# Performance work log

Hardware: AMD Instinct MI355X
Metric: run time of the kernel (lower is better)

Reference implementation:

```python
import jax, jax.numpy as jnp
import numpy as np

C_IN = 256
K = 4
C_QK = C_IN // K  # 64


def setup_inputs() -> dict:
    key = jax.random.key(0)
    ks = jax.random.split(key, 9)
    B, C, H, W = 4, C_IN, 64, 64
    s = 0.02
    return {
        "x": jax.random.normal(ks[0], (B, C, H, W), dtype=jnp.float32),
        # 1x1 convs stored as dense [out, in] matrices (kernel_size=1)
        "wq": jax.random.normal(ks[1], (C_QK, C), dtype=jnp.float32) * s,
        "bq": jax.random.normal(ks[2], (C_QK,), dtype=jnp.float32) * s,
        "wk": jax.random.normal(ks[3], (C_QK, C), dtype=jnp.float32) * s,
        "bk": jax.random.normal(ks[4], (C_QK,), dtype=jnp.float32) * s,
        "wv": jax.random.normal(ks[5], (C, C), dtype=jnp.float32) * s,
        "bv": jax.random.normal(ks[6], (C,), dtype=jnp.float32) * s,
        "wg": jax.random.normal(ks[7], (C, C), dtype=jnp.float32) * s,
        "bg": jax.random.normal(ks[8], (C,), dtype=jnp.float32) * s,
    }


def reference(x, wq, bq, wk, bk, wv, bv, wg, bg):
    B, C, H, W = x.shape
    N = H * W
    xf = x.reshape(B, C, N)  # [B, C, N]
    # 1x1 conv == per-pixel linear over channels
    q = jnp.einsum("oc,bcn->bon", wq, xf) + bq[None, :, None]  # [B, Cqk, N]
    k = jnp.einsum("oc,bcn->bon", wk, xf) + bk[None, :, None]  # [B, Cqk, N]
    v = jnp.einsum("oc,bcn->bon", wv, xf) + bv[None, :, None]  # [B, C, N]
    # energy[b, n, m] = <q[:, n], k[:, m]>  (n = query pos, m = key pos)
    energy = jnp.einsum("bon,bom->bnm", q, k)  # [B, N, N]
    energy = jax.nn.elu(energy) / N
    # out[b, c, m] = sum_n v[b, c, n] * energy[b, n, m]
    out = jnp.einsum("bcn,bnm->bcm", v, energy).reshape(B, C, H, W)
    out = jnp.einsum("oc,bchw->bohw", wg, out) + bg[None, :, None, None]
    return out
```

## Files before the change

### kernel.cpp

```cpp
#include <hip/hip_runtime.h>

#define B_ 4
#define C_ 256
#define CQK 64
#define N_ 4096
#define SEG 2
#define SEGN (N_ / SEG)
#define NB 128
#define ITERS (SEGN / NB)
#define TS 512

typedef _Float16 f16;
typedef __attribute__((ext_vector_type(8))) _Float16 f16x8;
typedef __attribute__((ext_vector_type(4))) _Float16 f16x4;
typedef __attribute__((ext_vector_type(4))) float f32x4;

#define TILE_OFF(l15, quad) ((l15) * 32 + (quad) * 8)

__global__ __launch_bounds__(256) void prep(
    const float* __restrict__ x, const float* __restrict__ wq,
    const float* __restrict__ wk, const float* __restrict__ wv,
    const float* __restrict__ wg, f16* __restrict__ xtt, f16* __restrict__ WQt,
    f16* __restrict__ WKt, f16* __restrict__ WVt, f16* __restrict__ WGt) {
  __shared__ float tile[64][65];
  if (blockIdx.x < 64) {
    int n0 = blockIdx.x * 64, c0 = blockIdx.y * 64, b = blockIdx.z;
    const float* xb = x + (size_t)b * C_ * N_;
    int lane = threadIdx.x & 63;
    int grp = threadIdx.x >> 6;
#pragma unroll
    for (int i = 0; i < 16; i++) {
      int c = grp * 16 + i;
      tile[lane][c] = xb[(size_t)(c0 + c) * N_ + n0 + lane];
    }
    __syncthreads();
    f16* xtb = xtt + (size_t)b * N_ * C_;
    int ti = threadIdx.x >> 6;
    int l15 = threadIdx.x & 15;
    int qq = (threadIdx.x >> 4) & 3;
    int nl = ti * 16 + l15;
    size_t tb = ((size_t)((n0 >> 4) + ti) * 8 + (c0 >> 5) + (qq >> 1)) * TS;
    f16* dst = xtb + tb + l15 * 32 + (qq & 1) * 16;
    f16x8 v0, v1;
#pragma unroll
    for (int j = 0; j < 8; j++) v0[j] = (f16)tile[nl][qq * 16 + j];
#pragma unroll
    for (int j = 0; j < 8; j++) v1[j] = (f16)tile[nl][qq * 16 + 8 + j];
    *(f16x8*)dst = v0;
    *(f16x8*)(dst + 8) = v1;
  } else {
    int wid = (((blockIdx.x - 64) * 16) + blockIdx.z * 4 + blockIdx.y) * 256 +
              threadIdx.x;
    for (int chunk = wid; chunk < 20480; chunk += 16384) {
      const float* src;
      f16* dst;
      int lo;
      if (chunk < 2048) { src = wq; dst = WQt; lo = chunk * 8; }
      else if (chunk < 4096) { src = wk; dst = WKt; lo = (chunk - 2048) * 8; }
      else if (chunk < 12288) { src = wv; dst = WVt; lo = (chunk - 4096) * 8; }
      else { src = wg; dst = WGt; lo = (chunk - 12288) * 8; }
      int o = lo >> 8, k = lo & 255;
      f16x8 v;
#pragma unroll
      for (int j = 0; j < 8; j++) v[j] = (f16)src[lo + j];
      *(f16x8*)(dst + ((size_t)(o >> 4) * 8 + (k >> 5)) * TS + (o & 15) * 32 +
                (k & 31)) = v;
    }
  }
}

__global__ __launch_bounds__(256) void proj_all(
    const f16* __restrict__ WQt, const f16* __restrict__ WKt,
    const f16* __restrict__ WVt, const float* __restrict__ bq,
    const float* __restrict__ bk, const float* __restrict__ bv,
    const f16* __restrict__ xtt, f16* __restrict__ QTt, f16* __restrict__ KTt,
    f16* __restrict__ Vt) {
  int n0 = blockIdx.x * 64;
  int y = blockIdx.y;
  int b = blockIdx.z;
  int tid = threadIdx.x, lane = tid & 63, w = tid >> 6;
  int l15 = lane & 15, quad = lane >> 4;
  const f16* xtb = xtt + (size_t)b * N_ * C_;
  if (y < 2) {
    const f16* Wt = y ? WKt : WQt;
    const float* bias = y ? bk : bq;
    f16* outT = y ? KTt : QTt;
    f32x4 acc[4];
#pragma unroll
    for (int nt = 0; nt < 4; nt++) acc[nt] = (f32x4){0.f, 0.f, 0.f, 0.f};
#pragma unroll
    for (int kt = 0; kt < 8; kt++) {
      f16x8 a = *(const f16x8*)(Wt + ((size_t)w * 8 + kt) * TS + TILE_OFF(l15, quad));
#pragma unroll
      for (int nt = 0; nt < 4; nt++) {
        f16x8 bf = *(const f16x8*)(xtb + ((size_t)((n0 >> 4) + nt) * 8 + kt) * TS +
                                   TILE_OFF(l15, quad));
        acc[nt] = __builtin_amdgcn_mfma_f32_16x16x32_f16(a, bf, acc[nt], 0, 0, 0);
      }
    }
    f16* ob = outT + (size_t)b * N_ * CQK;
    int o_lo = 16 * (w & 1) + 4 * quad;
    int okt = w >> 1;
#pragma unroll
    for (int nt = 0; nt < 4; nt++) {
      f16x4 vals;
#pragma unroll
      for (int r = 0; r < 4; r++)
        vals[r] = (f16)(acc[nt][r] + bias[16 * w + 4 * quad + r]);
      *(f16x4*)(ob + ((size_t)((n0 >> 4) + nt) * 2 + okt) * TS + l15 * 32 + o_lo) =
          vals;
    }
  } else {
    int o0 = (y - 2) * 64;
    f32x4 acc[4];
#pragma unroll
    for (int ot = 0; ot < 4; ot++) acc[ot] = (f32x4){0.f, 0.f, 0.f, 0.f};
#pragma unroll
    for (int kt = 0; kt < 8; kt++) {
      f16x8 a = *(const f16x8*)(xtb + ((size_t)((n0 >> 4) + w) * 8 + kt) * TS +
                                TILE_OFF(l15, quad));
#pragma unroll
      for (int ot = 0; ot < 4; ot++) {
        f16x8 bb = *(const f16x8*)(WVt + ((size_t)((o0 >> 4) + ot) * 8 + kt) * TS +
                                   TILE_OFF(l15, quad));
        acc[ot] = __builtin_amdgcn_mfma_f32_16x16x32_f16(a, bb, acc[ot], 0, 0, 0);
      }
    }
    f16* vbout = Vt + (size_t)b * C_ * N_;
    int n_lo = 16 * (w & 1) + 4 * quad;
    int ntile = (n0 >> 5) + (w >> 1);
#pragma unroll
    for (int ot = 0; ot < 4; ot++) {
      float bvv = bv[o0 + 16 * ot + l15];
      f16x4 vals;
#pragma unroll
      for (int r = 0; r < 4; r++) vals[r] = (f16)(acc[ot][r] + bvv);
      *(f16x4*)(vbout + ((size_t)((o0 >> 4) + ot) * 128 + ntile) * TS + l15 * 32 +
                n_lo) = vals;
    }
  }
}

__global__ __launch_bounds__(256, 2) void attn(const f16* __restrict__ qt,
                                               const f16* __restrict__ kt,
                                               const f16* __restrict__ v,
                                               f16* __restrict__ oT) {
  __shared__ __align__(16) f16 sPt[2][64][128];
  int m0 = blockIdx.x * 64;
  int seg = blockIdx.y;
  int b = blockIdx.z;
  int tid = threadIdx.x, lane = tid & 63, w = tid >> 6;
  int l15 = lane & 15, quad = lane >> 4;
  const f16* qtb = qt + (size_t)b * N_ * CQK;
  const f16* ktb = kt + (size_t)b * N_ * CQK;
  const f16* vb = v + (size_t)b * C_ * N_;

  f32x4 oacc[4][4];
#pragma unroll
  for (int ct = 0; ct < 4; ct++)
#pragma unroll
    for (int mt = 0; mt < 4; mt++) oacc[ct][mt] = (f32x4){0.f, 0.f, 0.f, 0.f};

  f16x8 kf[4][2];
#pragma unroll
  for (int mt = 0; mt < 4; mt++)
#pragma unroll
    for (int ks = 0; ks < 2; ks++)
      kf[mt][ks] = *(const f16x8*)(ktb + ((size_t)((m0 >> 4) + mt) * 2 + ks) * TS +
                                   TILE_OFF(l15, quad));

  f16x8 qf[2][2];
  {
    int nq = seg * SEGN;
#pragma unroll
    for (int nt = 0; nt < 2; nt++)
#pragma unroll
      for (int ks = 0; ks < 2; ks++)
        qf[nt][ks] = *(const f16x8*)(qtb +
                                     ((size_t)((nq >> 4) + 2 * w + nt) * 2 + ks) * TS +
                                     TILE_OFF(l15, quad));
  }

  for (int it = 0; it < ITERS; it++) {
    int n0 = seg * SEGN + it * NB;
    f16x8 vfA[2][4];
#pragma unroll
    for (int ks = 0; ks < 2; ks++)
#pragma unroll
      for (int ct = 0; ct < 4; ct++)
        vfA[ks][ct] = *(const f16x8*)(vb +
                                      ((size_t)(4 * w + ct) * 128 + (n0 >> 5) + ks) * TS +
                                      TILE_OFF(l15, quad));

    char* buf = (char*)sPt[it & 1];
#pragma unroll
    for (int nt = 0; nt < 2; nt++) {
      f32x4 sacc[4];
#pragma unroll
      for (int mt = 0; mt < 4; mt++) sacc[mt] = (f32x4){0.f, 0.f, 0.f, 0.f};
#pragma unroll
      for (int ks = 0; ks < 2; ks++)
#pragma unroll
        for (int mt = 0; mt < 4; mt++)
          sacc[mt] = __builtin_amdgcn_mfma_f32_16x16x32_f16(qf[nt][ks], kf[mt][ks],
                                                            sacc[mt], 0, 0, 0);
#pragma unroll
      for (int mt = 0; mt < 4; mt++) {
        f16x4 p;
#pragma unroll
        for (int r = 0; r < 4; r++) {
          float s = sacc[mt][r];
          p[r] = (f16)(s > 0.0f ? s : (__expf(s) - 1.0f));
        }
        int row = 16 * mt + l15;
        int colb = (64 * w + 32 * nt + 8 * quad) ^ ((row & 7) << 4);
        *(f16x4*)(buf + row * 256 + colb) = p;
      }
    }
    __syncthreads();

    f16x8 vfB[2][4];
    f16x8 pa[4];
#pragma unroll
    for (int mt = 0; mt < 4; mt++) {
      int row = 16 * mt + l15;
      int colb = (quad * 16) ^ ((row & 7) << 4);
      pa[mt] = *(const f16x8*)(buf + row * 256 + colb);
    }
#pragma unroll
    for (int ks = 0; ks < 2; ks++)
#pragma unroll
      for (int ct = 0; ct < 4; ct++)
        vfB[ks][ct] = *(const f16x8*)(vb + ((size_t)(4 * w + ct) * 128 + (n0 >> 5) +
                                            2 + ks) * TS +
                                      TILE_OFF(l15, quad));
#pragma unroll
    for (int ct = 0; ct < 4; ct++)
#pragma unroll
      for (int mt = 0; mt < 4; mt++)
        oacc[ct][mt] = __builtin_amdgcn_mfma_f32_16x16x32_f16(vfA[0][ct], pa[mt],
                                                              oacc[ct][mt], 0, 0, 0);
    if (it + 1 < ITERS) {
      int nq = n0 + NB;
#pragma unroll
      for (int nt = 0; nt < 2; nt++)
#pragma unroll
        for (int ks = 0; ks < 2; ks++)
          qf[nt][ks] = *(const f16x8*)(qtb +
                                       ((size_t)((nq >> 4) + 2 * w + nt) * 2 + ks) * TS +
                                       TILE_OFF(l15, quad));
    }
#pragma unroll
    for (int mt = 0; mt < 4; mt++) {
      int row = 16 * mt + l15;
      pa[mt] = *(const f16x8*)(buf + row * 256 + ((64 + quad * 16) ^ ((row & 7) << 4)));
    }
#pragma unroll
    for (int ct = 0; ct < 4; ct++)
#pragma unroll
      for (int mt = 0; mt < 4; mt++)
        oacc[ct][mt] = __builtin_amdgcn_mfma_f32_16x16x32_f16(vfA[1][ct], pa[mt],
                                                              oacc[ct][mt], 0, 0, 0);
#pragma unroll
    for (int mt = 0; mt < 4; mt++) {
      int row = 16 * mt + l15;
      pa[mt] = *(const f16x8*)(buf + row * 256 + ((128 + quad * 16) ^ ((row & 7) << 4)));
    }
#pragma unroll
    for (int ct = 0; ct < 4; ct++)
#pragma unroll
      for (int mt = 0; mt < 4; mt++)
        oacc[ct][mt] = __builtin_amdgcn_mfma_f32_16x16x32_f16(vfB[0][ct], pa[mt],
                                                              oacc[ct][mt], 0, 0, 0);
#pragma unroll
    for (int mt = 0; mt < 4; mt++) {
      int row = 16 * mt + l15;
      pa[mt] = *(const f16x8*)(buf + row * 256 + ((192 + quad * 16) ^ ((row & 7) << 4)));
    }
#pragma unroll
    for (int ct = 0; ct < 4; ct++)
#pragma unroll
      for (int mt = 0; mt < 4; mt++)
        oacc[ct][mt] = __builtin_amdgcn_mfma_f32_16x16x32_f16(vfB[1][ct], pa[mt],
                                                              oacc[ct][mt], 0, 0, 0);
  }

  f16* ob = oT + ((size_t)seg * B_ + b) * N_ * C_;
#pragma unroll
  for (int ct = 0; ct < 4; ct++) {
#pragma unroll
    for (int mt = 0; mt < 4; mt++) {
      f16x4 vals;
#pragma unroll
      for (int r = 0; r < 4; r++)
        vals[r] = (f16)(oacc[ct][mt][r] * (1.0f / (float)N_));
      size_t tb = ((size_t)((m0 >> 4) + mt) * 8 + 2 * w + (ct >> 1)) * TS;
      *(f16x4*)(ob + tb + l15 * 32 + 16 * (ct & 1) + 4 * quad) = vals;
    }
  }
}

__global__ __launch_bounds__(256) void final_proj(const f16* __restrict__ WGt,
                                                  const float* __restrict__ bias,
                                                  const f16* __restrict__ ot,
                                                  float* __restrict__ out) {
  int m0 = blockIdx.x * 64, o0 = blockIdx.y * 64, b = blockIdx.z;
  int tid = threadIdx.x, lane = tid & 63, w = tid >> 6;
  int l15 = lane & 15, quad = lane >> 4;
  const f16* otb0 = ot + (size_t)b * N_ * C_;
  const f16* otb1 = ot + ((size_t)B_ + b) * N_ * C_;
  f32x4 acc[4];
#pragma unroll
  for (int mt = 0; mt < 4; mt++) acc[mt] = (f32x4){0.f, 0.f, 0.f, 0.f};
#pragma unroll
  for (int kt = 0; kt < 8; kt++) {
    f16x8 a = *(const f16x8*)(WGt + ((size_t)((o0 >> 4) + w) * 8 + kt) * TS +
                              TILE_OFF(l15, quad));
#pragma unroll
    for (int mt = 0; mt < 4; mt++) {
      size_t off = ((size_t)((m0 >> 4) + mt) * 8 + kt) * TS + TILE_OFF(l15, quad);
      f16x8 b0 = *(const f16x8*)(otb0 + off);
      f16x8 b1 = *(const f16x8*)(otb1 + off);
      f16x8 bb = b0 + b1;
      acc[mt] = __builtin_amdgcn_mfma_f32_16x16x32_f16(a, bb, acc[mt], 0, 0, 0);
    }
  }
  float* outb = out + (size_t)b * C_ * N_;
  int ol = o0 + 16 * w + quad * 4;
#pragma unroll
  for (int mt = 0; mt < 4; mt++) {
    int m = m0 + 16 * mt + l15;
#pragma unroll
    for (int r = 0; r < 4; r++)
      outb[(size_t)(ol + r) * N_ + m] = acc[mt][r] + bias[ol + r];
  }
}

extern "C" void kernel_launch(void* const* d_in, const int* in_sizes, int n_in,
                              void* d_out, int out_size, void* d_ws, size_t ws_size,
                              hipStream_t stream) {
  const float* x = (const float*)d_in[0];
  const float* wq = (const float*)d_in[1];
  const float* bq = (const float*)d_in[2];
  const float* wk = (const float*)d_in[3];
  const float* bk = (const float*)d_in[4];
  const float* wv = (const float*)d_in[5];
  const float* bv = (const float*)d_in[6];
  const float* wg = (const float*)d_in[7];
  const float* bg = (const float*)d_in[8];
  float* out = (float*)d_out;

  char* ws = (char*)d_ws;
  f16* OTt = (f16*)ws;
  f16* XTt = (f16*)ws;
  ws += (size_t)SEG * B_ * N_ * C_ * sizeof(f16);
  f16* QTt = (f16*)ws; ws += (size_t)B_ * N_ * CQK * sizeof(f16);
  f16* KTt = (f16*)ws; ws += (size_t)B_ * N_ * CQK * sizeof(f16);
  f16* Vt  = (f16*)ws; ws += (size_t)B_ * C_ * N_ * sizeof(f16);
  f16* WQt = (f16*)ws; ws += (size_t)CQK * C_ * sizeof(f16);
  f16* WKt = (f16*)ws; ws += (size_t)CQK * C_ * sizeof(f16);
  f16* WVt = (f16*)ws; ws += (size_t)C_ * C_ * sizeof(f16);
  f16* WGt = (f16*)ws; ws += (size_t)C_ * C_ * sizeof(f16);

  prep<<<dim3(68, 4, 4), 256, 0, stream>>>(x, wq, wk, wv, wg, XTt, WQt, WKt, WVt, WGt);
  proj_all<<<dim3(N_ / 64, 6, B_), 256, 0, stream>>>(WQt, WKt, WVt, bq, bk, bv,
                                                     XTt, QTt, KTt, Vt);
  attn<<<dim3(N_ / 64, SEG, B_), 256, 0, stream>>>(QTt, KTt, Vt, OTt);
  final_proj<<<dim3(N_ / 64, C_ / 64, B_), 256, 0, stream>>>(WGt, bg, OTt, out);
}
```

Measured before the change: 172.8 us.

## Fuse transpose into projection and output projection into attention kernel

Replaces four launches with two. The fp32 transpose/cast of x moves into the projection kernel through shared memory, and one block now computes Q, K and V for its pixel tile. The attention kernel drops the split-N segmentation, halves its key-tile width to 32 so the grid stays large, and applies the wg output projection in-kernel from LDS. This removes the intermediate workspace round-trips and the segment-sum pass. In exchange, weights are converted from fp32 per block instead of once, and each attention block carries the full N loop with smaller MFMA tiles.

```diff
diff --git a/kernel.cpp b/kernel.cpp
--- a/kernel.cpp
+++ b/kernel.cpp
@@ -4,10 +4,8 @@
 #define C_ 256
 #define CQK 64
 #define N_ 4096
-#define SEG 2
-#define SEGN (N_ / SEG)
 #define NB 128
-#define ITERS (SEGN / NB)
+#define ITERS (N_ / NB)
 #define TS 512
 
 typedef _Float16 f16;
@@ -17,126 +15,105 @@
 
 #define TILE_OFF(l15, quad) ((l15) * 32 + (quad) * 8)
 
-__global__ __launch_bounds__(256) void prep(
+__global__ __launch_bounds__(256) void proj(
     const float* __restrict__ x, const float* __restrict__ wq,
-    const float* __restrict__ wk, const float* __restrict__ wv,
-    const float* __restrict__ wg, f16* __restrict__ xtt, f16* __restrict__ WQt,
-    f16* __restrict__ WKt, f16* __restrict__ WVt, f16* __restrict__ WGt) {
-  __shared__ float tile[64][65];
-  if (blockIdx.x < 64) {
-    int n0 = blockIdx.x * 64, c0 = blockIdx.y * 64, b = blockIdx.z;
-    const float* xb = x + (size_t)b * C_ * N_;
-    int lane = threadIdx.x & 63;
-    int grp = threadIdx.x >> 6;
-#pragma unroll
-    for (int i = 0; i < 16; i++) {
-      int c = grp * 16 + i;
-      tile[lane][c] = xb[(size_t)(c0 + c) * N_ + n0 + lane];
-    }
-    __syncthreads();
-    f16* xtb = xtt + (size_t)b * N_ * C_;
-    int ti = threadIdx.x >> 6;
-    int l15 = threadIdx.x & 15;
-    int qq = (threadIdx.x >> 4) & 3;
-    int nl = ti * 16 + l15;
-    size_t tb = ((size_t)((n0 >> 4) + ti) * 8 + (c0 >> 5) + (qq >> 1)) * TS;
-    f16* dst = xtb + tb + l15 * 32 + (qq & 1) * 16;
-    f16x8 v0, v1;
-#pragma unroll
-    for (int j = 0; j < 8; j++) v0[j] = (f16)tile[nl][qq * 16 + j];
-#pragma unroll
-    for (int j = 0; j < 8; j++) v1[j] = (f16)tile[nl][qq * 16 + 8 + j];
-    *(f16x8*)dst = v0;
-    *(f16x8*)(dst + 8) = v1;
-  } else {
-    int wid = (((blockIdx.x - 64) * 16) + blockIdx.z * 4 + blockIdx.y) * 256 +
-              threadIdx.x;
-    for (int chunk = wid; chunk < 20480; chunk += 16384) {
-      const float* src;
-      f16* dst;
-      int lo;
-      if (chunk < 2048) { src = wq; dst = WQt; lo = chunk * 8; }
-      else if (chunk < 4096) { src = wk; dst = WKt; lo = (chunk - 2048) * 8; }
-      else if (chunk < 12288) { src = wv; dst = WVt; lo = (chunk - 4096) * 8; }
-      else { src = wg; dst = WGt; lo = (chunk - 12288) * 8; }
-      int o = lo >> 8, k = lo & 255;
-      f16x8 v;
-#pragma unroll
-      for (int j = 0; j < 8; j++) v[j] = (f16)src[lo + j];
-      *(f16x8*)(dst + ((size_t)(o >> 4) * 8 + (k >> 5)) * TS + (o & 15) * 32 +
-                (k & 31)) = v;
-    }
-  }
-}
-
-__global__ __launch_bounds__(256) void proj_all(
-    const f16* __restrict__ WQt, const f16* __restrict__ WKt,
-    const f16* __restrict__ WVt, const float* __restrict__ bq,
-    const float* __restrict__ bk, const float* __restrict__ bv,
-    const f16* __restrict__ xtt, f16* __restrict__ QTt, f16* __restrict__ KTt,
+    const float* __restrict__ bq, const float* __restrict__ wk,
+    const float* __restrict__ bk, const float* __restrict__ wv,
+    const float* __restrict__ bv, f16* __restrict__ QTt, f16* __restrict__ KTt,
     f16* __restrict__ Vt) {
+  __shared__ float xs[64][65];
+  __shared__ f16 xt[4 * 8 * TS];
   int n0 = blockIdx.x * 64;
-  int y = blockIdx.y;
-  int b = blockIdx.z;
+  int b = blockIdx.y;
   int tid = threadIdx.x, lane = tid & 63, w = tid >> 6;
   int l15 = lane & 15, quad = lane >> 4;
-  const f16* xtb = xtt + (size_t)b * N_ * C_;
-  if (y < 2) {
-    const f16* Wt = y ? WKt : WQt;
-    const float* bias = y ? bk : bq;
-    f16* outT = y ? KTt : QTt;
-    f32x4 acc[4];
-#pragma unroll
-    for (int nt = 0; nt < 4; nt++) acc[nt] = (f32x4){0.f, 0.f, 0.f, 0.f};
-#pragma unroll
-    for (int kt = 0; kt < 8; kt++) {
-      f16x8 a = *(const f16x8*)(Wt + ((size_t)w * 8 + kt) * TS + TILE_OFF(l15, quad));
-#pragma unroll
-      for (int nt = 0; nt < 4; nt++) {
-        f16x8 bf = *(const f16x8*)(xtb + ((size_t)((n0 >> 4) + nt) * 8 + kt) * TS +
-                                   TILE_OFF(l15, quad));
-        acc[nt] = __builtin_amdgcn_mfma_f32_16x16x32_f16(a, bf, acc[nt], 0, 0, 0);
-      }
-    }
-    f16* ob = outT + (size_t)b * N_ * CQK;
-    int o_lo = 16 * (w & 1) + 4 * quad;
-    int okt = w >> 1;
+  const float* xb = x + (size_t)b * C_ * N_;
+
+  for (int cc = 0; cc < 4; cc++) {
+#pragma unroll
+    for (int i = 0; i < 16; i++)
+      xs[lane][w * 16 + i] = xb[(size_t)(cc * 64 + w * 16 + i) * N_ + n0 + lane];
+    __syncthreads();
+    {
+      int nt = w;
+      f16x8 v0, v1;
+#pragma unroll
+      for (int j = 0; j < 8; j++) v0[j] = (f16)xs[nt * 16 + l15][quad * 16 + j];
+#pragma unroll
+      for (int j = 0; j < 8; j++) v1[j] = (f16)xs[nt * 16 + l15][quad * 16 + 8 + j];
+      f16* dst = xt + (nt * 8 + cc * 2 + (quad >> 1)) * TS + l15 * 32 + (quad & 1) * 16;
+      *(f16x8*)dst = v0;
+      *(f16x8*)(dst + 8) = v1;
+    }
+    __syncthreads();
+  }
+
+  const float* wqk = (w < 2) ? wq : wk;
+  const float* bqk = (w < 2) ? bq : bk;
+  f32x4 accV[4][4];
+  f32x4 accQ[2][4];
+#pragma unroll
+  for (int ot = 0; ot < 4; ot++)
+#pragma unroll
+    for (int nt = 0; nt < 4; nt++) accV[ot][nt] = (f32x4){0.f, 0.f, 0.f, 0.f};
+#pragma unroll
+  for (int ot = 0; ot < 2; ot++)
+#pragma unroll
+    for (int nt = 0; nt < 4; nt++) accQ[ot][nt] = (f32x4){0.f, 0.f, 0.f, 0.f};
+
+#pragma unroll
+  for (int kt = 0; kt < 8; kt++) {
+    f16x8 xf[4];
+#pragma unroll
+    for (int nt = 0; nt < 4; nt++)
+      xf[nt] = *(const f16x8*)(xt + (nt * 8 + kt) * TS + TILE_OFF(l15, quad));
+#pragma unroll
+    for (int ot = 0; ot < 4; ot++) {
+      const float* p = wv + (size_t)(64 * w + 16 * ot + l15) * C_ + kt * 32 + quad * 8;
+      f16x8 bf;
+#pragma unroll
+      for (int j = 0; j < 8; j++) bf[j] = (f16)p[j];
+#pragma unroll
+      for (int nt = 0; nt < 4; nt++)
+        accV[ot][nt] = __builtin_amdgcn_mfma_f32_16x16x32_f16(xf[nt], bf, accV[ot][nt], 0, 0, 0);
+    }
+#pragma unroll
+    for (int ot = 0; ot < 2; ot++) {
+      const float* p = wqk + (size_t)(32 * (w & 1) + 16 * ot + l15) * C_ + kt * 32 + quad * 8;
+      f16x8 af;
+#pragma unroll
+      for (int j = 0; j < 8; j++) af[j] = (f16)p[j];
+#pragma unroll
+      for (int nt = 0; nt < 4; nt++)
+        accQ[ot][nt] = __builtin_amdgcn_mfma_f32_16x16x32_f16(af, xf[nt], accQ[ot][nt], 0, 0, 0);
+    }
+  }
+
+  f16* vbout = Vt + (size_t)b * C_ * N_;
+#pragma unroll
+  for (int ot = 0; ot < 4; ot++) {
+    int o = 64 * w + 16 * ot + l15;
+    float bvv = bv[o];
 #pragma unroll
     for (int nt = 0; nt < 4; nt++) {
       f16x4 vals;
 #pragma unroll
+      for (int r = 0; r < 4; r++) vals[r] = (f16)(accV[ot][nt][r] + bvv);
+      *(f16x4*)(vbout + ((size_t)(4 * w + ot) * 128 + (n0 >> 5) + (nt >> 1)) * TS +
+                l15 * 32 + 16 * (nt & 1) + 4 * quad) = vals;
+    }
+  }
+  f16* ob = ((w < 2) ? QTt : KTt) + (size_t)b * N_ * CQK;
+#pragma unroll
+  for (int ot = 0; ot < 2; ot++) {
+#pragma unroll
+    for (int nt = 0; nt < 4; nt++) {
+      f16x4 vals;
+#pragma unroll
       for (int r = 0; r < 4; r++)
-        vals[r] = (f16)(acc[nt][r] + bias[16 * w + 4 * quad + r]);
-      *(f16x4*)(ob + ((size_t)((n0 >> 4) + nt) * 2 + okt) * TS + l15 * 32 + o_lo) =
-          vals;
-    }
-  } else {
-    int o0 = (y - 2) * 64;
-    f32x4 acc[4];
-#pragma unroll
-    for (int ot = 0; ot < 4; ot++) acc[ot] = (f32x4){0.f, 0.f, 0.f, 0.f};
-#pragma unroll
-    for (int kt = 0; kt < 8; kt++) {
-      f16x8 a = *(const f16x8*)(xtb + ((size_t)((n0 >> 4) + w) * 8 + kt) * TS +
-                                TILE_OFF(l15, quad));
-#pragma unroll
-      for (int ot = 0; ot < 4; ot++) {
-        f16x8 bb = *(const f16x8*)(WVt + ((size_t)((o0 >> 4) + ot) * 8 + kt) * TS +
-                                   TILE_OFF(l15, quad));
-        acc[ot] = __builtin_amdgcn_mfma_f32_16x16x32_f16(a, bb, acc[ot], 0, 0, 0);
-      }
-    }
-    f16* vbout = Vt + (size_t)b * C_ * N_;
-    int n_lo = 16 * (w & 1) + 4 * quad;
-    int ntile = (n0 >> 5) + (w >> 1);
-#pragma unroll
-    for (int ot = 0; ot < 4; ot++) {
-      float bvv = bv[o0 + 16 * ot + l15];
-      f16x4 vals;
-#pragma unroll
-      for (int r = 0; r < 4; r++) vals[r] = (f16)(acc[ot][r] + bvv);
-      *(f16x4*)(vbout + ((size_t)((o0 >> 4) + ot) * 128 + ntile) * TS + l15 * 32 +
-                n_lo) = vals;
+        vals[r] = (f16)(accQ[ot][nt][r] + bqk[32 * (w & 1) + 16 * ot + 4 * quad + r]);
+      *(f16x4*)(ob + (((size_t)(n0 >> 4) + nt) * 2 + (w & 1)) * TS + l15 * 32 +
+                16 * ot + 4 * quad) = vals;
     }
   }
 }
@@ -144,45 +121,42 @@
 __global__ __launch_bounds__(256, 2) void attn(const f16* __restrict__ qt,
                                                const f16* __restrict__ kt,
                                                const f16* __restrict__ v,
-                                               f16* __restrict__ oT) {
-  __shared__ __align__(16) f16 sPt[2][64][128];
-  int m0 = blockIdx.x * 64;
-  int seg = blockIdx.y;
-  int b = blockIdx.z;
+                                               const float* __restrict__ wg,
+                                               const float* __restrict__ bg,
+                                               float* __restrict__ out) {
+  __shared__ __align__(16) f16 sPt[2][32][128];
+  int m0 = blockIdx.x * 32;
+  int b = blockIdx.y;
   int tid = threadIdx.x, lane = tid & 63, w = tid >> 6;
   int l15 = lane & 15, quad = lane >> 4;
   const f16* qtb = qt + (size_t)b * N_ * CQK;
   const f16* ktb = kt + (size_t)b * N_ * CQK;
   const f16* vb = v + (size_t)b * C_ * N_;
 
-  f32x4 oacc[4][4];
+  f32x4 oacc[4][2];
 #pragma unroll
   for (int ct = 0; ct < 4; ct++)
 #pragma unroll
-    for (int mt = 0; mt < 4; mt++) oacc[ct][mt] = (f32x4){0.f, 0.f, 0.f, 0.f};
-
-  f16x8 kf[4][2];
-#pragma unroll
-  for (int mt = 0; mt < 4; mt++)
+    for (int mt = 0; mt < 2; mt++) oacc[ct][mt] = (f32x4){0.f, 0.f, 0.f, 0.f};
+
+  f16x8 kf[2][2];
+#pragma unroll
+  for (int mt = 0; mt < 2; mt++)
 #pragma unroll
     for (int ks = 0; ks < 2; ks++)
       kf[mt][ks] = *(const f16x8*)(ktb + ((size_t)((m0 >> 4) + mt) * 2 + ks) * TS +
                                    TILE_OFF(l15, quad));
 
   f16x8 qf[2][2];
-  {
-    int nq = seg * SEGN;
-#pragma unroll
-    for (int nt = 0; nt < 2; nt++)
-#pragma unroll
-      for (int ks = 0; ks < 2; ks++)
-        qf[nt][ks] = *(const f16x8*)(qtb +
-                                     ((size_t)((nq >> 4) + 2 * w + nt) * 2 + ks) * TS +
-                                     TILE_OFF(l15, quad));
-  }
+#pragma unroll
+  for (int nt = 0; nt < 2; nt++)
+#pragma unroll
+    for (int ks = 0; ks < 2; ks++)
+      qf[nt][ks] = *(const f16x8*)(qtb + ((size_t)(2 * w + nt) * 2 + ks) * TS +
+                                   TILE_OFF(l15, quad));
 
   for (int it = 0; it < ITERS; it++) {
-    int n0 = seg * SEGN + it * NB;
+    int n0 = it * NB;
     f16x8 vfA[2][4];
 #pragma unroll
     for (int ks = 0; ks < 2; ks++)
@@ -195,17 +169,17 @@
     char* buf = (char*)sPt[it & 1];
 #pragma unroll
     for (int nt = 0; nt < 2; nt++) {
-      f32x4 sacc[4];
-#pragma unroll
-      for (int mt = 0; mt < 4; mt++) sacc[mt] = (f32x4){0.f, 0.f, 0.f, 0.f};
+      f32x4 sacc[2];
+#pragma unroll
+      for (int mt = 0; mt < 2; mt++) sacc[mt] = (f32x4){0.f, 0.f, 0.f, 0.f};
 #pragma unroll
       for (int ks = 0; ks < 2; ks++)
 #pragma unroll
-        for (int mt = 0; mt < 4; mt++)
+        for (int mt = 0; mt < 2; mt++)
           sacc[mt] = __builtin_amdgcn_mfma_f32_16x16x32_f16(qf[nt][ks], kf[mt][ks],
                                                             sacc[mt], 0, 0, 0);
 #pragma unroll
-      for (int mt = 0; mt < 4; mt++) {
+      for (int mt = 0; mt < 2; mt++) {
         f16x4 p;
 #pragma unroll
         for (int r = 0; r < 4; r++) {
@@ -220,12 +194,11 @@
     __syncthreads();
 
     f16x8 vfB[2][4];
-    f16x8 pa[4];
-#pragma unroll
-    for (int mt = 0; mt < 4; mt++) {
+    f16x8 pa[2];
+#pragma unroll
+    for (int mt = 0; mt < 2; mt++) {
       int row = 16 * mt + l15;
-      int colb = (quad * 16) ^ ((row & 7) << 4);
-      pa[mt] = *(const f16x8*)(buf + row * 256 + colb);
+      pa[mt] = *(const f16x8*)(buf + row * 256 + ((quad * 16) ^ ((row & 7) << 4)));
     }
 #pragma unroll
     for (int ks = 0; ks < 2; ks++)
@@ -237,7 +210,7 @@
 #pragma unroll
     for (int ct = 0; ct < 4; ct++)
 #pragma unroll
-      for (int mt = 0; mt < 4; mt++)
+      for (int mt = 0; mt < 2; mt++)
         oacc[ct][mt] = __builtin_amdgcn_mfma_f32_16x16x32_f16(vfA[0][ct], pa[mt],
                                                               oacc[ct][mt], 0, 0, 0);
     if (it + 1 < ITERS) {
@@ -251,88 +224,89 @@
                                        TILE_OFF(l15, quad));
     }
 #pragma unroll
-    for (int mt = 0; mt < 4; mt++) {
+    for (int mt = 0; mt < 2; mt++) {
       int row = 16 * mt + l15;
       pa[mt] = *(const f16x8*)(buf + row * 256 + ((64 + quad * 16) ^ ((row & 7) << 4)));
     }
 #pragma unroll
     for (int ct = 0; ct < 4; ct++)
 #pragma unroll
-      for (int mt = 0; mt < 4; mt++)
+      for (int mt = 0; mt < 2; mt++)
         oacc[ct][mt] = __builtin_amdgcn_mfma_f32_16x16x32_f16(vfA[1][ct], pa[mt],
                                                               oacc[ct][mt], 0, 0, 0);
 #pragma unroll
-    for (int mt = 0; mt < 4; mt++) {
+    for (int mt = 0; mt < 2; mt++) {
       int row = 16 * mt + l15;
       pa[mt] = *(const f16x8*)(buf + row * 256 + ((128 + quad * 16) ^ ((row & 7) << 4)));
     }
 #pragma unroll
     for (int ct = 0; ct < 4; ct++)
 #pragma unroll
-      for (int mt = 0; mt < 4; mt++)
+      for (int mt = 0; mt < 2; mt++)
         oacc[ct][mt] = __builtin_amdgcn_mfma_f32_16x16x32_f16(vfB[0][ct], pa[mt],
                                                               oacc[ct][mt], 0, 0, 0);
 #pragma unroll
-    for (int mt = 0; mt < 4; mt++) {
+    for (int mt = 0; mt < 2; mt++) {
       int row = 16 * mt + l15;
       pa[mt] = *(const f16x8*)(buf + row * 256 + ((192 + quad * 16) ^ ((row & 7) << 4)));
     }
 #pragma unroll
     for (int ct = 0; ct < 4; ct++)
 #pragma unroll
-      for (int mt = 0; mt < 4; mt++)
+      for (int mt = 0; mt < 2; mt++)
         oacc[ct][mt] = __builtin_amdgcn_mfma_f32_16x16x32_f16(vfB[1][ct], pa[mt],
                                                               oacc[ct][mt], 0, 0, 0);
   }
 
-  f16* ob = oT + ((size_t)seg * B_ + b) * N_ * C_;
+  __syncthreads();
+  f16* obuf = (f16*)sPt;
 #pragma unroll
   for (int ct = 0; ct < 4; ct++) {
 #pragma unroll
-    for (int mt = 0; mt < 4; mt++) {
+    for (int mt = 0; mt < 2; mt++) {
       f16x4 vals;
 #pragma unroll
       for (int r = 0; r < 4; r++)
         vals[r] = (f16)(oacc[ct][mt][r] * (1.0f / (float)N_));
-      size_t tb = ((size_t)((m0 >> 4) + mt) * 8 + 2 * w + (ct >> 1)) * TS;
-      *(f16x4*)(ob + tb + l15 * 32 + 16 * (ct & 1) + 4 * quad) = vals;
-    }
-  }
-}
-
-__global__ __launch_bounds__(256) void final_proj(const f16* __restrict__ WGt,
-                                                  const float* __restrict__ bias,
-                                                  const f16* __restrict__ ot,
-                                                  float* __restrict__ out) {
-  int m0 = blockIdx.x * 64, o0 = blockIdx.y * 64, b = blockIdx.z;
-  int tid = threadIdx.x, lane = tid & 63, w = tid >> 6;
-  int l15 = lane & 15, quad = lane >> 4;
-  const f16* otb0 = ot + (size_t)b * N_ * C_;
-  const f16* otb1 = ot + ((size_t)B_ + b) * N_ * C_;
-  f32x4 acc[4];
-#pragma unroll
-  for (int mt = 0; mt < 4; mt++) acc[mt] = (f32x4){0.f, 0.f, 0.f, 0.f};
+      *(f16x4*)(obuf + (mt * 8 + 2 * w + (ct >> 1)) * TS + l15 * 32 +
+                16 * (ct & 1) + 4 * quad) = vals;
+    }
+  }
+  __syncthreads();
+  f32x4 accO[4][2];
+#pragma unroll
+  for (int ot = 0; ot < 4; ot++)
+#pragma unroll
+    for (int mt = 0; mt < 2; mt++) accO[ot][mt] = (f32x4){0.f, 0.f, 0.f, 0.f};
 #pragma unroll
   for (int kt = 0; kt < 8; kt++) {
-    f16x8 a = *(const f16x8*)(WGt + ((size_t)((o0 >> 4) + w) * 8 + kt) * TS +
-                              TILE_OFF(l15, quad));
-#pragma unroll
-    for (int mt = 0; mt < 4; mt++) {
-      size_t off = ((size_t)((m0 >> 4) + mt) * 8 + kt) * TS + TILE_OFF(l15, quad);
-      f16x8 b0 = *(const f16x8*)(otb0 + off);
-      f16x8 b1 = *(const f16x8*)(otb1 + off);
-      f16x8 bb = b0 + b1;
-      acc[mt] = __builtin_amdgcn_mfma_f32_16x16x32_f16(a, bb, acc[mt], 0, 0, 0);
+    f16x8 bO[2];
+#pragma unroll
+    for (int mt = 0; mt < 2; mt++)
+      bO[mt] = *(const f16x8*)(obuf + (mt * 8 + kt) * TS + TILE_OFF(l15, quad));
+#pragma unroll
+    for (int ot = 0; ot < 4; ot++) {
+      const float* p = wg + (size_t)(64 * w + 16 * ot + l15) * C_ + kt * 32 + quad * 8;
+      f16x8 af;
+#pragma unroll
+      for (int j = 0; j < 8; j++) af[j] = (f16)p[j];
+#pragma unroll
+      for (int mt = 0; mt < 2; mt++)
+        accO[ot][mt] = __builtin_amdgcn_mfma_f32_16x16x32_f16(af, bO[mt], accO[ot][mt], 0, 0, 0);
     }
   }
   float* outb = out + (size_t)b * C_ * N_;
-  int ol = o0 + 16 * w + quad * 4;
-#pragma unroll
-  for (int mt = 0; mt < 4; mt++) {
-    int m = m0 + 16 * mt + l15;
-#pragma unroll
-    for (int r = 0; r < 4; r++)
-      outb[(size_t)(ol + r) * N_ + m] = acc[mt][r] + bias[ol + r];
+#pragma unroll
+  for (int ot = 0; ot < 4; ot++) {
+#pragma unroll
+    for (int mt = 0; mt < 2; mt++) {
+      int m = m0 + 16 * mt + l15;
+#pragma unroll
+      for (int r = 0; r < 4; r++) {
+        int o = 64 * w + 16 * ot + 4 * quad + r;
+        outb[(size_t)o * N_ + m] = accO[ot][mt][r] + bg[o];
+      }
+    }
   }
 }
 
@@ -351,20 +325,11 @@
   float* out = (float*)d_out;
 
   char* ws = (char*)d_ws;
-  f16* OTt = (f16*)ws;
-  f16* XTt = (f16*)ws;
-  ws += (size_t)SEG * B_ * N_ * C_ * sizeof(f16);
   f16* QTt = (f16*)ws; ws += (size_t)B_ * N_ * CQK * sizeof(f16);
   f16* KTt = (f16*)ws; ws += (size_t)B_ * N_ * CQK * sizeof(f16);
   f16* Vt  = (f16*)ws; ws += (size_t)B_ * C_ * N_ * sizeof(f16);
-  f16* WQt = (f16*)ws; ws += (size_t)CQK * C_ * sizeof(f16);
-  f16* WKt = (f16*)ws; ws += (size_t)CQK * C_ * sizeof(f16);
-  f16* WVt = (f16*)ws; ws += (size_t)C_ * C_ * sizeof(f16);
-  f16* WGt = (f16*)ws; ws += (size_t)C_ * C_ * sizeof(f16);
-
-  prep<<<dim3(68, 4, 4), 256, 0, stream>>>(x, wq, wk, wv, wg, XTt, WQt, WKt, WVt, WGt);
-  proj_all<<<dim3(N_ / 64, 6, B_), 256, 0, stream>>>(WQt, WKt, WVt, bq, bk, bv,
-                                                     XTt, QTt, KTt, Vt);
-  attn<<<dim3(N_ / 64, SEG, B_), 256, 0, stream>>>(QTt, KTt, Vt, OTt);
-  final_proj<<<dim3(N_ / 64, C_ / 64, B_), 256, 0, stream>>>(WGt, bg, OTt, out);
+
+  proj<<<dim3(N_ / 64, B_), 256, 0, stream>>>(x, wq, bq, wk, bk, wv, bv,
+                                              QTt, KTt, Vt);
+  attn<<<dim3(N_ / 32, B_), 256, 0, stream>>>(QTt, KTt, Vt, wg, bg, out);
 }
```

After: 202.1 us. +17.0%, slower.

## Fuse x transpose into projection and output projection into attention epilogue

Applied to the files above, without the earlier changes.

Splits weight conversion into its own small kernel, and moves the x transpose/f16 conversion into the projection kernel via shared memory. All Q, K and V tiles are now computed per 512-thread block, so the f16 transposed copy of x is no longer written to or read from global memory. The Wg projection is applied inside the attention epilogue on each segment's output, producing fp32 partials that a combine kernel sums and biases. This removes the intermediate f16 attention-output round trip and the separate final GEMM. In exchange it writes two full fp32 partial tensors and adds one more elementwise pass.

```diff
diff --git a/kernel.cpp b/kernel.cpp
--- a/kernel.cpp
+++ b/kernel.cpp
@@ -14,129 +14,118 @@
 typedef __attribute__((ext_vector_type(8))) _Float16 f16x8;
 typedef __attribute__((ext_vector_type(4))) _Float16 f16x4;
 typedef __attribute__((ext_vector_type(4))) float f32x4;
+typedef __attribute__((ext_vector_type(4))) float float4v;
 
 #define TILE_OFF(l15, quad) ((l15) * 32 + (quad) * 8)
 
-__global__ __launch_bounds__(256) void prep(
-    const float* __restrict__ x, const float* __restrict__ wq,
-    const float* __restrict__ wk, const float* __restrict__ wv,
-    const float* __restrict__ wg, f16* __restrict__ xtt, f16* __restrict__ WQt,
-    f16* __restrict__ WKt, f16* __restrict__ WVt, f16* __restrict__ WGt) {
-  __shared__ float tile[64][65];
-  if (blockIdx.x < 64) {
-    int n0 = blockIdx.x * 64, c0 = blockIdx.y * 64, b = blockIdx.z;
-    const float* xb = x + (size_t)b * C_ * N_;
-    int lane = threadIdx.x & 63;
-    int grp = threadIdx.x >> 6;
-#pragma unroll
-    for (int i = 0; i < 16; i++) {
-      int c = grp * 16 + i;
-      tile[lane][c] = xb[(size_t)(c0 + c) * N_ + n0 + lane];
-    }
-    __syncthreads();
-    f16* xtb = xtt + (size_t)b * N_ * C_;
-    int ti = threadIdx.x >> 6;
-    int l15 = threadIdx.x & 15;
-    int qq = (threadIdx.x >> 4) & 3;
-    int nl = ti * 16 + l15;
-    size_t tb = ((size_t)((n0 >> 4) + ti) * 8 + (c0 >> 5) + (qq >> 1)) * TS;
-    f16* dst = xtb + tb + l15 * 32 + (qq & 1) * 16;
-    f16x8 v0, v1;
-#pragma unroll
-    for (int j = 0; j < 8; j++) v0[j] = (f16)tile[nl][qq * 16 + j];
-#pragma unroll
-    for (int j = 0; j < 8; j++) v1[j] = (f16)tile[nl][qq * 16 + 8 + j];
-    *(f16x8*)dst = v0;
-    *(f16x8*)(dst + 8) = v1;
-  } else {
-    int wid = (((blockIdx.x - 64) * 16) + blockIdx.z * 4 + blockIdx.y) * 256 +
-              threadIdx.x;
-    for (int chunk = wid; chunk < 20480; chunk += 16384) {
-      const float* src;
-      f16* dst;
-      int lo;
-      if (chunk < 2048) { src = wq; dst = WQt; lo = chunk * 8; }
-      else if (chunk < 4096) { src = wk; dst = WKt; lo = (chunk - 2048) * 8; }
-      else if (chunk < 12288) { src = wv; dst = WVt; lo = (chunk - 4096) * 8; }
-      else { src = wg; dst = WGt; lo = (chunk - 12288) * 8; }
-      int o = lo >> 8, k = lo & 255;
-      f16x8 v;
-#pragma unroll
-      for (int j = 0; j < 8; j++) v[j] = (f16)src[lo + j];
-      *(f16x8*)(dst + ((size_t)(o >> 4) * 8 + (k >> 5)) * TS + (o & 15) * 32 +
-                (k & 31)) = v;
-    }
-  }
-}
-
-__global__ __launch_bounds__(256) void proj_all(
-    const f16* __restrict__ WQt, const f16* __restrict__ WKt,
-    const f16* __restrict__ WVt, const float* __restrict__ bq,
-    const float* __restrict__ bk, const float* __restrict__ bv,
-    const f16* __restrict__ xtt, f16* __restrict__ QTt, f16* __restrict__ KTt,
+__global__ __launch_bounds__(256) void prep_w(
+    const float* __restrict__ wq, const float* __restrict__ wk,
+    const float* __restrict__ wv, const float* __restrict__ wg,
+    f16* __restrict__ WQt, f16* __restrict__ WKt, f16* __restrict__ WVt,
+    f16* __restrict__ WGt) {
+  int chunk = blockIdx.x * 256 + threadIdx.x;
+  if (chunk >= 20480) return;
+  const float* src;
+  f16* dst;
+  int lo;
+  if (chunk < 2048) { src = wq; dst = WQt; lo = chunk * 8; }
+  else if (chunk < 4096) { src = wk; dst = WKt; lo = (chunk - 2048) * 8; }
+  else if (chunk < 12288) { src = wv; dst = WVt; lo = (chunk - 4096) * 8; }
+  else { src = wg; dst = WGt; lo = (chunk - 12288) * 8; }
+  int o = lo >> 8, k = lo & 255;
+  f16x8 v;
+#pragma unroll
+  for (int j = 0; j < 8; j++) v[j] = (f16)src[lo + j];
+  *(f16x8*)(dst + ((size_t)(o >> 4) * 8 + (k >> 5)) * TS + (o & 15) * 32 + (k & 31)) = v;
+}
+
+__global__ __launch_bounds__(512) void proj(
+    const float* __restrict__ x, const f16* __restrict__ WQt,
+    const f16* __restrict__ WKt, const f16* __restrict__ WVt,
+    const float* __restrict__ bq, const float* __restrict__ bk,
+    const float* __restrict__ bv, f16* __restrict__ QTt, f16* __restrict__ KTt,
     f16* __restrict__ Vt) {
+  __shared__ float xs[64][65];
+  __shared__ f16 xt[4 * 8 * TS];
   int n0 = blockIdx.x * 64;
-  int y = blockIdx.y;
-  int b = blockIdx.z;
+  int b = blockIdx.y;
   int tid = threadIdx.x, lane = tid & 63, w = tid >> 6;
   int l15 = lane & 15, quad = lane >> 4;
-  const f16* xtb = xtt + (size_t)b * N_ * C_;
-  if (y < 2) {
-    const f16* Wt = y ? WKt : WQt;
-    const float* bias = y ? bk : bq;
-    f16* outT = y ? KTt : QTt;
-    f32x4 acc[4];
-#pragma unroll
-    for (int nt = 0; nt < 4; nt++) acc[nt] = (f32x4){0.f, 0.f, 0.f, 0.f};
-#pragma unroll
-    for (int kt = 0; kt < 8; kt++) {
-      f16x8 a = *(const f16x8*)(Wt + ((size_t)w * 8 + kt) * TS + TILE_OFF(l15, quad));
+  const float* xb = x + (size_t)b * C_ * N_;
+
+  for (int cc = 0; cc < 4; cc++) {
+#pragma unroll
+    for (int i = 0; i < 8; i++)
+      xs[lane][w * 8 + i] = xb[(size_t)(cc * 64 + w * 8 + i) * N_ + n0 + lane];
+    __syncthreads();
+    {
+      int nt = w >> 1;
+      f16x8 v;
+#pragma unroll
+      for (int j = 0; j < 8; j++)
+        v[j] = (f16)xs[nt * 16 + l15][32 * (w & 1) + quad * 8 + j];
+      *(f16x8*)(xt + (nt * 8 + cc * 2 + (w & 1)) * TS + l15 * 32 + quad * 8) = v;
+    }
+    __syncthreads();
+  }
+
+  f32x4 acc[3][4];
+#pragma unroll
+  for (int j = 0; j < 3; j++)
+#pragma unroll
+    for (int nt = 0; nt < 4; nt++) acc[j][nt] = (f32x4){0.f, 0.f, 0.f, 0.f};
+
+#pragma unroll
+  for (int kt = 0; kt < 8; kt++) {
+    f16x8 xf[4];
+#pragma unroll
+    for (int nt = 0; nt < 4; nt++)
+      xf[nt] = *(const f16x8*)(xt + (nt * 8 + kt) * TS + TILE_OFF(l15, quad));
+#pragma unroll
+    for (int j = 0; j < 3; j++) {
+      int g = w * 3 + j;
+      const f16* Wt;
+      int ot;
+      bool isV = g < 16;
+      if (isV) { Wt = WVt; ot = g; }
+      else if (g < 20) { Wt = WQt; ot = g - 16; }
+      else { Wt = WKt; ot = g - 20; }
+      f16x8 wf = *(const f16x8*)(Wt + ((size_t)ot * 8 + kt) * TS + TILE_OFF(l15, quad));
+#pragma unroll
+      for (int nt = 0; nt < 4; nt++)
+        acc[j][nt] = isV
+            ? __builtin_amdgcn_mfma_f32_16x16x32_f16(xf[nt], wf, acc[j][nt], 0, 0, 0)
+            : __builtin_amdgcn_mfma_f32_16x16x32_f16(wf, xf[nt], acc[j][nt], 0, 0, 0);
+    }
+  }
+
+  f16* vbout = Vt + (size_t)b * C_ * N_;
+#pragma unroll
+  for (int j = 0; j < 3; j++) {
+    int g = w * 3 + j;
+    if (g < 16) {
+      float bvv = bv[16 * g + l15];
 #pragma unroll
       for (int nt = 0; nt < 4; nt++) {
-        f16x8 bf = *(const f16x8*)(xtb + ((size_t)((n0 >> 4) + nt) * 8 + kt) * TS +
-                                   TILE_OFF(l15, quad));
-        acc[nt] = __builtin_amdgcn_mfma_f32_16x16x32_f16(a, bf, acc[nt], 0, 0, 0);
+        f16x4 vals;
+#pragma unroll
+        for (int r = 0; r < 4; r++) vals[r] = (f16)(acc[j][nt][r] + bvv);
+        *(f16x4*)(vbout + ((size_t)g * 128 + (n0 >> 5) + (nt >> 1)) * TS +
+                  l15 * 32 + 16 * (nt & 1) + 4 * quad) = vals;
       }
-    }
-    f16* ob = outT + (size_t)b * N_ * CQK;
-    int o_lo = 16 * (w & 1) + 4 * quad;
-    int okt = w >> 1;
-#pragma unroll
-    for (int nt = 0; nt < 4; nt++) {
-      f16x4 vals;
-#pragma unroll
-      for (int r = 0; r < 4; r++)
-        vals[r] = (f16)(acc[nt][r] + bias[16 * w + 4 * quad + r]);
-      *(f16x4*)(ob + ((size_t)((n0 >> 4) + nt) * 2 + okt) * TS + l15 * 32 + o_lo) =
-          vals;
-    }
-  } else {
-    int o0 = (y - 2) * 64;
-    f32x4 acc[4];
-#pragma unroll
-    for (int ot = 0; ot < 4; ot++) acc[ot] = (f32x4){0.f, 0.f, 0.f, 0.f};
-#pragma unroll
-    for (int kt = 0; kt < 8; kt++) {
-      f16x8 a = *(const f16x8*)(xtb + ((size_t)((n0 >> 4) + w) * 8 + kt) * TS +
-                                TILE_OFF(l15, quad));
-#pragma unroll
-      for (int ot = 0; ot < 4; ot++) {
-        f16x8 bb = *(const f16x8*)(WVt + ((size_t)((o0 >> 4) + ot) * 8 + kt) * TS +
-                                   TILE_OFF(l15, quad));
-        acc[ot] = __builtin_amdgcn_mfma_f32_16x16x32_f16(a, bb, acc[ot], 0, 0, 0);
+    } else {
+      int oq = (g < 20) ? (g - 16) : (g - 20);
+      const float* bias = (g < 20) ? bq : bk;
+      f16* ob = ((g < 20) ? QTt : KTt) + (size_t)b * N_ * CQK;
+#pragma unroll
+      for (int nt = 0; nt < 4; nt++) {
+        f16x4 vals;
+#pragma unroll
+        for (int r = 0; r < 4; r++)
+          vals[r] = (f16)(acc[j][nt][r] + bias[16 * oq + 4 * quad + r]);
+        *(f16x4*)(ob + (((size_t)(n0 >> 4) + nt) * 2 + (oq >> 1)) * TS + l15 * 32 +
+                  16 * (oq & 1) + 4 * quad) = vals;
       }
-    }
-    f16* vbout = Vt + (size_t)b * C_ * N_;
-    int n_lo = 16 * (w & 1) + 4 * quad;
-    int ntile = (n0 >> 5) + (w >> 1);
-#pragma unroll
-    for (int ot = 0; ot < 4; ot++) {
-      float bvv = bv[o0 + 16 * ot + l15];
-      f16x4 vals;
-#pragma unroll
-      for (int r = 0; r < 4; r++) vals[r] = (f16)(acc[ot][r] + bvv);
-      *(f16x4*)(vbout + ((size_t)((o0 >> 4) + ot) * 128 + ntile) * TS + l15 * 32 +
-                n_lo) = vals;
     }
   }
 }
@@ -144,7 +133,8 @@
 __global__ __launch_bounds__(256, 2) void attn(const f16* __restrict__ qt,
                                                const f16* __restrict__ kt,
                                                const f16* __restrict__ v,
-                                               f16* __restrict__ oT) {
+                                               const f16* __restrict__ WGt,
+                                               float* __restrict__ part) {
   __shared__ __align__(16) f16 sPt[2][64][128];
   int m0 = blockIdx.x * 64;
   int seg = blockIdx.y;
@@ -224,8 +214,7 @@
 #pragma unroll
     for (int mt = 0; mt < 4; mt++) {
       int row = 16 * mt + l15;
-      int colb = (quad * 16) ^ ((row & 7) << 4);
-      pa[mt] = *(const f16x8*)(buf + row * 256 + colb);
+      pa[mt] = *(const f16x8*)(buf + row * 256 + ((quad * 16) ^ ((row & 7) << 4)));
     }
 #pragma unroll
     for (int ks = 0; ks < 2; ks++)
@@ -285,7 +274,8 @@
                                                               oacc[ct][mt], 0, 0, 0);
   }
 
-  f16* ob = oT + ((size_t)seg * B_ + b) * N_ * C_;
+  __syncthreads();
+  f16* obuf = (f16*)sPt;
 #pragma unroll
   for (int ct = 0; ct < 4; ct++) {
 #pragma unroll
@@ -294,46 +284,56 @@
 #pragma unroll
       for (int r = 0; r < 4; r++)
         vals[r] = (f16)(oacc[ct][mt][r] * (1.0f / (float)N_));
-      size_t tb = ((size_t)((m0 >> 4) + mt) * 8 + 2 * w + (ct >> 1)) * TS;
-      *(f16x4*)(ob + tb + l15 * 32 + 16 * (ct & 1) + 4 * quad) = vals;
-    }
-  }
-}
-
-__global__ __launch_bounds__(256) void final_proj(const f16* __restrict__ WGt,
-                                                  const float* __restrict__ bias,
-                                                  const f16* __restrict__ ot,
-                                                  float* __restrict__ out) {
-  int m0 = blockIdx.x * 64, o0 = blockIdx.y * 64, b = blockIdx.z;
-  int tid = threadIdx.x, lane = tid & 63, w = tid >> 6;
-  int l15 = lane & 15, quad = lane >> 4;
-  const f16* otb0 = ot + (size_t)b * N_ * C_;
-  const f16* otb1 = ot + ((size_t)B_ + b) * N_ * C_;
-  f32x4 acc[4];
-#pragma unroll
-  for (int mt = 0; mt < 4; mt++) acc[mt] = (f32x4){0.f, 0.f, 0.f, 0.f};
+      *(f16x4*)(obuf + (mt * 8 + 2 * w + (ct >> 1)) * TS + l15 * 32 +
+                16 * (ct & 1) + 4 * quad) = vals;
+    }
+  }
+  __syncthreads();
+  f32x4 accO[4][4];
+#pragma unroll
+  for (int ot = 0; ot < 4; ot++)
+#pragma unroll
+    for (int mt = 0; mt < 4; mt++) accO[ot][mt] = (f32x4){0.f, 0.f, 0.f, 0.f};
 #pragma unroll
   for (int kt = 0; kt < 8; kt++) {
-    f16x8 a = *(const f16x8*)(WGt + ((size_t)((o0 >> 4) + w) * 8 + kt) * TS +
-                              TILE_OFF(l15, quad));
-#pragma unroll
-    for (int mt = 0; mt < 4; mt++) {
-      size_t off = ((size_t)((m0 >> 4) + mt) * 8 + kt) * TS + TILE_OFF(l15, quad);
-      f16x8 b0 = *(const f16x8*)(otb0 + off);
-      f16x8 b1 = *(const f16x8*)(otb1 + off);
-      f16x8 bb = b0 + b1;
-      acc[mt] = __builtin_amdgcn_mfma_f32_16x16x32_f16(a, bb, acc[mt], 0, 0, 0);
-    }
-  }
-  float* outb = out + (size_t)b * C_ * N_;
-  int ol = o0 + 16 * w + quad * 4;
-#pragma unroll
-  for (int mt = 0; mt < 4; mt++) {
-    int m = m0 + 16 * mt + l15;
-#pragma unroll
-    for (int r = 0; r < 4; r++)
-      outb[(size_t)(ol + r) * N_ + m] = acc[mt][r] + bias[ol + r];
-  }
+    f16x8 bO[4];
+#pragma unroll
+    for (int mt = 0; mt < 4; mt++)
+      bO[mt] = *(const f16x8*)(obuf + (mt * 8 + kt) * TS + TILE_OFF(l15, quad));
+#pragma unroll
+    for (int ot = 0; ot < 4; ot++) {
+      f16x8 af = *(const f16x8*)(WGt + ((size_t)(4 * w + ot) * 8 + kt) * TS +
+                                 TILE_OFF(l15, quad));
+#pragma unroll
+      for (int mt = 0; mt < 4; mt++)
+        accO[ot][mt] = __builtin_amdgcn_mfma_f32_16x16x32_f16(af, bO[mt], accO[ot][mt], 0, 0, 0);
+    }
+  }
+  float* pb = part + ((size_t)(seg * B_ + b) * C_) * N_;
+#pragma unroll
+  for (int ot = 0; ot < 4; ot++) {
+#pragma unroll
+    for (int mt = 0; mt < 4; mt++) {
+      int m = m0 + 16 * mt + l15;
+#pragma unroll
+      for (int r = 0; r < 4; r++) {
+        int o = 64 * w + 16 * ot + 4 * quad + r;
+        pb[(size_t)o * N_ + m] = accO[ot][mt][r];
+      }
+    }
+  }
+}
+
+__global__ __launch_bounds__(256) void combine(const float* __restrict__ part,
+                                               const float* __restrict__ bg,
+                                               float* __restrict__ out) {
+  size_t i = ((size_t)blockIdx.x * 256 + threadIdx.x) * 4;
+  float4v p0 = *(const float4v*)(part + i);
+  float4v p1 = *(const float4v*)(part + (size_t)B_ * C_ * N_ + i);
+  float bgo = bg[(i >> 12) & 255];
+  float4v r = p0 + p1;
+  r[0] += bgo; r[1] += bgo; r[2] += bgo; r[3] += bgo;
+  *(float4v*)(out + i) = r;
 }
 
 extern "C" void kernel_launch(void* const* d_in, const int* in_sizes, int n_in,
@@ -351,9 +351,6 @@
   float* out = (float*)d_out;
 
   char* ws = (char*)d_ws;
-  f16* OTt = (f16*)ws;
-  f16* XTt = (f16*)ws;
-  ws += (size_t)SEG * B_ * N_ * C_ * sizeof(f16);
   f16* QTt = (f16*)ws; ws += (size_t)B_ * N_ * CQK * sizeof(f16);
   f16* KTt = (f16*)ws; ws += (size_t)B_ * N_ * CQK * sizeof(f16);
   f16* Vt  = (f16*)ws; ws += (size_t)B_ * C_ * N_ * sizeof(f16);
@@ -361,10 +358,11 @@
   f16* WKt = (f16*)ws; ws += (size_t)CQK * C_ * sizeof(f16);
   f16* WVt = (f16*)ws; ws += (size_t)C_ * C_ * sizeof(f16);
   f16* WGt = (f16*)ws; ws += (size_t)C_ * C_ * sizeof(f16);
-
-  prep<<<dim3(68, 4, 4), 256, 0, stream>>>(x, wq, wk, wv, wg, XTt, WQt, WKt, WVt, WGt);
-  proj_all<<<dim3(N_ / 64, 6, B_), 256, 0, stream>>>(WQt, WKt, WVt, bq, bk, bv,
-                                                     XTt, QTt, KTt, Vt);
-  attn<<<dim3(N_ / 64, SEG, B_), 256, 0, stream>>>(QTt, KTt, Vt, OTt);
-  final_proj<<<dim3(N_ / 64, C_ / 64, B_), 256, 0, stream>>>(WGt, bg, OTt, out);
-}
+  float* PART = (float*)ws; ws += (size_t)SEG * B_ * C_ * N_ * sizeof(float);
+
+  prep_w<<<dim3(80), 256, 0, stream>>>(wq, wk, wv, wg, WQt, WKt, WVt, WGt);
+  proj<<<dim3(N_ / 64, B_), 512, 0, stream>>>(x, WQt, WKt, WVt, bq, bk, bv,
+                                              QTt, KTt, Vt);
+  attn<<<dim3(N_ / 64, SEG, B_), 256, 0, stream>>>(QTt, KTt, Vt, WGt, PART);
+  combine<<<dim3(4096), 256, 0, stream>>>(PART, bg, out);
+}
```

Measured after the change: 161.2 us. 1.07x faster.
